# Optimization experiments

Measured on AMD Instinct MI355X. Metric: run time of the kernel, lower is better.

## Reference

```python
import jax, jax.numpy as jnp
import numpy as np


def bilinear_sampler(img, flow):
    """Warp img (B,H,W,C) by per-pixel flow (B,H,W,2): sample at (x+u, y+v).
    Border handling: indices clipped to the image (edge padding)."""
    B, H, W, C = img.shape
    gy, gx = jnp.meshgrid(jnp.arange(H, dtype=img.dtype),
                          jnp.arange(W, dtype=img.dtype), indexing='ij')
    x = gx[None] + flow[..., 0]  # (B,H,W)
    y = gy[None] + flow[..., 1]
    x0f = jnp.floor(x)
    y0f = jnp.floor(y)
    wx = x - x0f  # fractional parts, differentiable w.r.t. flow
    wy = y - y0f
    x0 = jnp.clip(x0f.astype(jnp.int32), 0, W - 1)
    x1 = jnp.clip(x0f.astype(jnp.int32) + 1, 0, W - 1)
    y0 = jnp.clip(y0f.astype(jnp.int32), 0, H - 1)
    y1 = jnp.clip(y0f.astype(jnp.int32) + 1, 0, H - 1)
    b = jnp.arange(B)[:, None, None]
    Ia = img[b, y0, x0]  # (B,H,W,C)
    Ib = img[b, y1, x0]
    Ic = img[b, y0, x1]
    Id = img[b, y1, x1]
    wx = wx[..., None]
    wy = wy[..., None]
    return (Ia * (1 - wx) * (1 - wy) + Ib * (1 - wx) * wy
            + Ic * wx * (1 - wy) + Id * wx * wy)


def setup_inputs() -> dict:
    key = jax.random.key(0)
    k1, k2, k3, k4, k5, k6 = jax.random.split(key, 6)
    B, H, W = 8, 512, 512
    return {
        't': jax.random.uniform(k1, (B, 1, 1, 1), dtype=jnp.float32),
        'I0': jax.random.uniform(k2, (B, H, W, 3), dtype=jnp.float32),
        'I1': jax.random.uniform(k3, (B, H, W, 3), dtype=jnp.float32),
        'interp': jax.random.normal(k4, (B, H, W, 5), dtype=jnp.float32),
        'Fhat_t0': jax.random.normal(k5, (B, H, W, 2), dtype=jnp.float32),
        'Fhat_t1': jax.random.normal(k6, (B, H, W, 2), dtype=jnp.float32),
    }


def reference(t, I0, I1, interp, Fhat_t0, Fhat_t1):
    Ft0 = interp[..., 0:2] + Fhat_t0
    Ft1 = interp[..., 2:4] + Fhat_t1
    Vt0 = jax.nn.sigmoid(interp[..., 4:5])  # (B,H,W,1) -> broadcasts over RGB
    Vt1 = 1.0 - Vt0
    g0 = bilinear_sampler(I0, Ft0)
    g1 = bilinear_sampler(I1, Ft1)
    eps = 1e-12
    w0 = (1.0 - t) * Vt0
    w1 = t * Vt1
    It = (w0 * g0 + w1 * g1) / (w0 + w1 + eps)
    return It
```

## Files before the change

kernel.cpp:

```cpp
#include <hip/hip_runtime.h>

constexpr int B_ = 8;
constexpr int H_ = 512;
constexpr int W_ = 512;
constexpr int HW_ = H_ * W_;

constexpr int TS = 32;
constexpr int R_ = 8;
constexpr int RS = TS + 2 * R_;
constexpr int RROW = RS * 3;
constexpr int NSPX = RS * RS;

__device__ __forceinline__ void sampleT(const float* __restrict__ lds,
                                        const float* __restrict__ img,
                                        int gx0, int gy0,
                                        float sx, float sy, float g[3]) {
    float xf = floorf(sx), yf = floorf(sy);
    float wx = sx - xf, wy = sy - yf;
    int ix = (int)xf, iy = (int)yf;
    int x0 = min(max(ix, 0), W_ - 1);
    int x1 = min(max(ix + 1, 0), W_ - 1);
    int y0 = min(max(iy, 0), H_ - 1);
    int y1 = min(max(iy + 1, 0), H_ - 1);

    float w00 = (1.0f - wx) * (1.0f - wy);
    float w01 = wx * (1.0f - wy);
    float w10 = (1.0f - wx) * wy;
    float w11 = wx * wy;

    int lx0 = x0 - gx0, lx1 = x1 - gx0;
    int ly0 = y0 - gy0, ly1 = y1 - gy0;
    bool inT = ((unsigned)lx0 < (unsigned)RS) & ((unsigned)lx1 < (unsigned)RS) &
               ((unsigned)ly0 < (unsigned)RS) & ((unsigned)ly1 < (unsigned)RS);

    if (inT) {
        const float* a = lds + ly0 * RROW;
        const float* c = lds + ly1 * RROW;
        int o0 = lx0 * 3, o1 = lx1 * 3;
        #pragma unroll
        for (int ch = 0; ch < 3; ++ch)
            g[ch] = a[o0 + ch] * w00 + a[o1 + ch] * w01 +
                    c[o0 + ch] * w10 + c[o1 + ch] * w11;
    } else {
        const float* pa = img + ((size_t)y0 * W_ + x0) * 3;
        const float* pb = img + ((size_t)y0 * W_ + x1) * 3;
        const float* pc = img + ((size_t)y1 * W_ + x0) * 3;
        const float* pd = img + ((size_t)y1 * W_ + x1) * 3;
        #pragma unroll
        for (int ch = 0; ch < 3; ++ch)
            g[ch] = pa[ch] * w00 + pb[ch] * w01 +
                    pc[ch] * w10 + pd[ch] * w11;
    }
}

__global__ __launch_bounds__(256) void frame_interp_tiled(
    const float* __restrict__ t,
    const float* __restrict__ I0,
    const float* __restrict__ I1,
    const float* __restrict__ interp,
    const float* __restrict__ F0,
    const float* __restrict__ F1,
    float* __restrict__ out)
{
    __shared__ float lds0[RS * RROW];
    __shared__ float lds1[RS * RROW];

    int tid = threadIdx.x;
    int bid = blockIdx.x;
    int b    = bid & 7;
    int tile = bid >> 3;
    int ty   = tile >> 4;
    int tx   = tile & 15;
    int gx0 = tx * TS - R_;
    int gy0 = ty * TS - R_;

    const float* img0 = I0 + (size_t)b * HW_ * 3;
    const float* img1 = I1 + (size_t)b * HW_ * 3;

    #pragma unroll
    for (int k = 0; k < NSPX / 256; ++k) {
        int p  = tid + k * 256;
        int ry = p / RS;
        int pu = p - ry * RS;
        int gy = min(max(gy0 + ry, 0), H_ - 1);
        int gx = min(max(gx0 + pu, 0), W_ - 1);
        size_t s = ((size_t)gy * W_ + gx) * 3;
        int d = p * 3;
        lds0[d + 0] = img0[s + 0];
        lds0[d + 1] = img0[s + 1];
        lds0[d + 2] = img0[s + 2];
        lds1[d + 0] = img1[s + 0];
        lds1[d + 1] = img1[s + 1];
        lds1[d + 2] = img1[s + 2];
    }
    __syncthreads();

    float tb = t[b];

    #pragma unroll
    for (int k = 0; k < 4; ++k) {
        int p   = tid + k * 256;
        int row = p >> 5;
        int col = p & 31;
        int gx = tx * TS + col;
        int gy = ty * TS + row;
        int idx = b * HW_ + gy * W_ + gx;

        const float* ip  = interp + (size_t)idx * 5;
        float i0 = ip[0], i1 = ip[1], i2 = ip[2], i3 = ip[3], i4 = ip[4];
        const float* f0p = F0 + (size_t)idx * 2;
        const float* f1p = F1 + (size_t)idx * 2;

        float ft0x = i0 + f0p[0];
        float ft0y = i1 + f0p[1];
        float ft1x = i2 + f1p[0];
        float ft1y = i3 + f1p[1];
        float vt0  = 1.0f / (1.0f + __expf(-i4));

        float g0[3], g1[3];
        sampleT(lds0, img0, gx0, gy0, (float)gx + ft0x, (float)gy + ft0y, g0);
        sampleT(lds1, img1, gx0, gy0, (float)gx + ft1x, (float)gy + ft1y, g1);

        float w0 = (1.0f - tb) * vt0;
        float w1 = tb * (1.0f - vt0);
        float inv = 1.0f / (w0 + w1 + 1e-12f);

        float* op = out + (size_t)idx * 3;
        op[0] = (w0 * g0[0] + w1 * g1[0]) * inv;
        op[1] = (w0 * g0[1] + w1 * g1[1]) * inv;
        op[2] = (w0 * g0[2] + w1 * g1[2]) * inv;
    }
}

extern "C" void kernel_launch(void* const* d_in, const int* in_sizes, int n_in,
                              void* d_out, int out_size, void* d_ws, size_t ws_size,
                              hipStream_t stream) {
    const float* t      = (const float*)d_in[0];
    const float* I0     = (const float*)d_in[1];
    const float* I1     = (const float*)d_in[2];
    const float* interp = (const float*)d_in[3];
    const float* F0     = (const float*)d_in[4];
    const float* F1     = (const float*)d_in[5];
    float* out = (float*)d_out;

    int blocks = B_ * (H_ / TS) * (W_ / TS);
    frame_interp_tiled<<<blocks, 256, 0, stream>>>(t, I0, I1, interp, F0, F1, out);
}
```

Measured before the change: 164.9 us.

## Store LDS image tiles as fp16 half2 and interpolate with packed half math

Converts the staged image halos to fp16, stored as RG and B(padded) half2 arrays, and does the bilinear blend with packed half2 FMAs. The halo radius drops from 8 to 6 and launch bounds now request more blocks per CU, to cut LDS footprint and raise occupancy. Global loads and stores are merged into wider memcpy accesses. The cost is fp16 precision in the interpolation and more samples falling back to slow global gathers because of the smaller halo.

Measured after the change: 164.4 us. Within noise of the previous version (-0.3%).

```diff
diff --git a/kernel.cpp b/kernel.cpp
--- a/kernel.cpp
+++ b/kernel.cpp
@@ -1,4 +1,5 @@
 #include <hip/hip_runtime.h>
+#include <hip/hip_fp16.h>
 
 constexpr int B_ = 8;
 constexpr int H_ = 512;
@@ -6,12 +7,13 @@
 constexpr int HW_ = H_ * W_;
 
 constexpr int TS = 32;
-constexpr int R_ = 8;
+constexpr int R_ = 6;
 constexpr int RS = TS + 2 * R_;
-constexpr int RROW = RS * 3;
 constexpr int NSPX = RS * RS;
 
-__device__ __forceinline__ void sampleT(const float* __restrict__ lds,
+
+__device__ __forceinline__ void sampleT(const __half2* __restrict__ rgp,
+                                        const __half2* __restrict__ bp,
                                         const float* __restrict__ img,
                                         int gx0, int gy0,
                                         float sx, float sy, float g[3]) {
@@ -34,13 +36,23 @@
                ((unsigned)ly0 < (unsigned)RS) & ((unsigned)ly1 < (unsigned)RS);
 
     if (inT) {
-        const float* a = lds + ly0 * RROW;
-        const float* c = lds + ly1 * RROW;
-        int o0 = lx0 * 3, o1 = lx1 * 3;
-        #pragma unroll
-        for (int ch = 0; ch < 3; ++ch)
-            g[ch] = a[o0 + ch] * w00 + a[o1 + ch] * w01 +
-                    c[o0 + ch] * w10 + c[o1 + ch] * w11;
+        int p00 = ly0 * RS + lx0, p01 = ly0 * RS + lx1;
+        int p10 = ly1 * RS + lx0, p11 = ly1 * RS + lx1;
+        __half2 h00 = __float2half2_rn(w00);
+        __half2 h01 = __float2half2_rn(w01);
+        __half2 h10 = __float2half2_rn(w10);
+        __half2 h11 = __float2half2_rn(w11);
+        __half2 rg = __hmul2(h00, rgp[p00]);
+        rg = __hfma2(h01, rgp[p01], rg);
+        rg = __hfma2(h10, rgp[p10], rg);
+        rg = __hfma2(h11, rgp[p11], rg);
+        __half2 bb = __hmul2(h00, bp[p00]);
+        bb = __hfma2(h01, bp[p01], bb);
+        bb = __hfma2(h10, bp[p10], bb);
+        bb = __hfma2(h11, bp[p11], bb);
+        g[0] = __low2float(rg);
+        g[1] = __high2float(rg);
+        g[2] = __low2float(bb);
     } else {
         const float* pa = img + ((size_t)y0 * W_ + x0) * 3;
         const float* pb = img + ((size_t)y0 * W_ + x1) * 3;
@@ -53,7 +65,7 @@
     }
 }
 
-__global__ __launch_bounds__(256) void frame_interp_tiled(
+__global__ __launch_bounds__(256, 5) void frame_interp_tiled(
     const float* __restrict__ t,
     const float* __restrict__ I0,
     const float* __restrict__ I1,
@@ -62,8 +74,8 @@
     const float* __restrict__ F1,
     float* __restrict__ out)
 {
-    __shared__ float lds0[RS * RROW];
-    __shared__ float lds1[RS * RROW];
+    __shared__ __half2 lds_rg[2][NSPX];
+    __shared__ __half2 lds_b[2][NSPX];
 
     int tid = threadIdx.x;
     int bid = blockIdx.x;
@@ -78,20 +90,22 @@
     const float* img1 = I1 + (size_t)b * HW_ * 3;
 
     #pragma unroll
-    for (int k = 0; k < NSPX / 256; ++k) {
-        int p  = tid + k * 256;
-        int ry = p / RS;
-        int pu = p - ry * RS;
-        int gy = min(max(gy0 + ry, 0), H_ - 1);
-        int gx = min(max(gx0 + pu, 0), W_ - 1);
-        size_t s = ((size_t)gy * W_ + gx) * 3;
-        int d = p * 3;
-        lds0[d + 0] = img0[s + 0];
-        lds0[d + 1] = img0[s + 1];
-        lds0[d + 2] = img0[s + 2];
-        lds1[d + 0] = img1[s + 0];
-        lds1[d + 1] = img1[s + 1];
-        lds1[d + 2] = img1[s + 2];
+    for (int k = 0; k < (NSPX + 255) / 256; ++k) {
+        int p = tid + k * 256;
+        if (p < NSPX) {
+            int ry = p / RS;
+            int rx = p - ry * RS;
+            int gy = min(max(gy0 + ry, 0), H_ - 1);
+            int gx = min(max(gx0 + rx, 0), W_ - 1);
+            size_t s = ((size_t)gy * W_ + gx) * 3;
+            float c0[3], c1[3];
+            __builtin_memcpy(c0, img0 + s, 12);
+            __builtin_memcpy(c1, img1 + s, 12);
+            lds_rg[0][p] = __floats2half2_rn(c0[0], c0[1]);
+            lds_b[0][p]  = __floats2half2_rn(c0[2], 0.0f);
+            lds_rg[1][p] = __floats2half2_rn(c1[0], c1[1]);
+            lds_b[1][p]  = __floats2half2_rn(c1[2], 0.0f);
+        }
     }
     __syncthreads();
 
@@ -106,29 +120,35 @@
         int gy = ty * TS + row;
         int idx = b * HW_ + gy * W_ + gx;
 
-        const float* ip  = interp + (size_t)idx * 5;
-        float i0 = ip[0], i1 = ip[1], i2 = ip[2], i3 = ip[3], i4 = ip[4];
-        const float* f0p = F0 + (size_t)idx * 2;
-        const float* f1p = F1 + (size_t)idx * 2;
+        const float* ip = interp + (size_t)idx * 5;
+        float i01[2], i23[2];
+        __builtin_memcpy(i01, ip, 8);
+        __builtin_memcpy(i23, ip + 2, 8);
+        float i4 = ip[4];
+        float2 f0 = *(const float2*)(F0 + (size_t)idx * 2);
+        float2 f1 = *(const float2*)(F1 + (size_t)idx * 2);
 
-        float ft0x = i0 + f0p[0];
-        float ft0y = i1 + f0p[1];
-        float ft1x = i2 + f1p[0];
-        float ft1y = i3 + f1p[1];
+        float ft0x = i01[0] + f0.x;
+        float ft0y = i01[1] + f0.y;
+        float ft1x = i23[0] + f1.x;
+        float ft1y = i23[1] + f1.y;
         float vt0  = 1.0f / (1.0f + __expf(-i4));
 
         float g0[3], g1[3];
-        sampleT(lds0, img0, gx0, gy0, (float)gx + ft0x, (float)gy + ft0y, g0);
-        sampleT(lds1, img1, gx0, gy0, (float)gx + ft1x, (float)gy + ft1y, g1);
+        sampleT(lds_rg[0], lds_b[0], img0, gx0, gy0,
+                (float)gx + ft0x, (float)gy + ft0y, g0);
+        sampleT(lds_rg[1], lds_b[1], img1, gx0, gy0,
+                (float)gx + ft1x, (float)gy + ft1y, g1);
 
         float w0 = (1.0f - tb) * vt0;
         float w1 = tb * (1.0f - vt0);
         float inv = 1.0f / (w0 + w1 + 1e-12f);
 
-        float* op = out + (size_t)idx * 3;
-        op[0] = (w0 * g0[0] + w1 * g1[0]) * inv;
-        op[1] = (w0 * g0[1] + w1 * g1[1]) * inv;
-        op[2] = (w0 * g0[2] + w1 * g1[2]) * inv;
+        float o[3];
+        o[0] = (w0 * g0[0] + w1 * g1[0]) * inv;
+        o[1] = (w0 * g0[1] + w1 * g1[1]) * inv;
+        o[2] = (w0 * g0[2] + w1 * g1[2]) * inv;
+        __builtin_memcpy(out + (size_t)idx * 3, o, 12);
     }
 }
 
```
